# Performance work log

Measured on AMD Instinct MI355X. Metric: run time of the kernel, lower is better.

## Reference

```python
import jax, jax.numpy as jnp
import numpy as np

CUTOFF = 10.0
EPS_W = 1e-5
EPS_LN = 1e-5

def _silu(v):
    return v * jax.nn.sigmoid(v)

def setup_inputs() -> dict:
    key = jax.random.key(0)
    ks = jax.random.split(key, 12)
    N, E, H, R = 50000, 300000, 256, 64
    s = lambda fan_in: 1.0 / np.sqrt(fan_in)
    inp = {
        'x': jax.random.normal(ks[0], (N, H), jnp.float32),
        'edge_index': jax.random.randint(ks[1], (2, E), 0, N, jnp.int64 if jax.config.jax_enable_x64 else jnp.int32),
        'distances': jax.random.uniform(ks[2], (E,), jnp.float32) * CUTOFF,
        'centers': jnp.linspace(0.0, CUTOFF, R).astype(jnp.float32),
        'widths': jnp.full((R,), CUTOFF / R, jnp.float32),
        'rbf_w1': jax.random.normal(ks[3], (R, R), jnp.float32) * s(R),
        'rbf_b1': jnp.zeros((R,), jnp.float32),
        'rbf_w2': jax.random.normal(ks[4], (R, R), jnp.float32) * s(R),
        'rbf_b2': jnp.zeros((R,), jnp.float32),
        'filt_w1': jax.random.normal(ks[5], (R, H), jnp.float32) * s(R),
        'filt_b1': jnp.zeros((H,), jnp.float32),
        'filt_w2': jax.random.normal(ks[6], (H, H), jnp.float32) * s(H),
        'filt_b2': jnp.zeros((H,), jnp.float32),
        'filt_w3': jax.random.normal(ks[7], (H, H), jnp.float32) * s(H),
        'filt_b3': jnp.zeros((H,), jnp.float32),
        'node_w': jax.random.normal(ks[8], (H, H), jnp.float32) * s(H),
        'node_b': jnp.zeros((H,), jnp.float32),
        'ln_g': jnp.ones((H,), jnp.float32),
        'ln_b': jnp.zeros((H,), jnp.float32),
        'gate_w': jax.random.normal(ks[9], (H, H), jnp.float32) * s(H),
        'gate_b': jnp.zeros((H,), jnp.float32),
    }
    return inp

def reference(x, edge_index, distances, centers, widths,
              rbf_w1, rbf_b1, rbf_w2, rbf_b2,
              filt_w1, filt_b1, filt_w2, filt_b2, filt_w3, filt_b3,
              node_w, node_b, ln_g, ln_b, gate_w, gate_b):
    # LearnableRBF: envelope * gaussian basis, then 2-layer SiLU proj
    d = distances
    env = 0.5 * (jnp.cos(d * jnp.pi / CUTOFF) + 1.0) * (d < CUTOFF).astype(x.dtype)  # [E]
    rbf = jnp.exp(-0.5 * ((d[:, None] - centers) / (jnp.abs(widths) + EPS_W)) ** 2)   # [E,R]
    r = rbf * env[:, None]
    r = _silu(r @ rbf_w1 + rbf_b1) @ rbf_w2 + rbf_b2                                  # [E,R]
    # filter network: Lin-SiLU-Lin-SiLU-Lin
    W = _silu(r @ filt_w1 + filt_b1)
    W = _silu(W @ filt_w2 + filt_b2) @ filt_w3 + filt_b3                              # [E,H]
    # gather -> modulate -> scatter-add (CFConv messaging)
    row, col = edge_index[0], edge_index[1]
    msg = (x[col] @ node_w + node_b) * W                                              # [E,H]
    agg = jax.ops.segment_sum(msg, row, num_segments=x.shape[0])                      # [N,H]
    h = x + agg
    mu = jnp.mean(h, axis=-1, keepdims=True)
    var = jnp.var(h, axis=-1, keepdims=True)
    out = (h - mu) / jnp.sqrt(var + EPS_LN) * ln_g + ln_b
    return out * jax.nn.sigmoid(out @ gate_w + gate_b)
```

## Files before the change

### kernel.cpp

```cpp
#include <hip/hip_runtime.h>
#include <hip/hip_bf16.h>
#include <math.h>

typedef __attribute__((ext_vector_type(8))) short bf16x8;
typedef __attribute__((ext_vector_type(4))) float f32x4;
typedef unsigned short ushort_t;

constexpr float F_CUTOFF = 10.0f;
constexpr float F_EPS_W  = 1e-5f;
constexpr float F_EPS_LN = 1e-5f;
constexpr float F_PI     = 3.14159265358979323846f;

__device__ __forceinline__ float silu_f(float v)   { return v / (1.0f + __expf(-v)); }
__device__ __forceinline__ float sigmoid_f(float v){ return 1.0f / (1.0f + __expf(-v)); }

__device__ __forceinline__ ushort_t f2bf(float f) {
    union { __hip_bfloat16 h; ushort_t u; } v; v.h = __float2bfloat16(f); return v.u;
}
__device__ __forceinline__ float bf2f(ushort_t u) {
    union { unsigned u; float f; } v; v.u = ((unsigned)u) << 16; return v.f;
}

__device__ __forceinline__ float f4c(const float4& v, int q) {
    return q == 0 ? v.x : q == 1 ? v.y : q == 2 ? v.z : v.w;
}

__global__ void count_kernel(const int* __restrict__ eidx, int* __restrict__ cnt, int E)
{
    int e = blockIdx.x * 256 + threadIdx.x;
    if (e < E) atomicAdd(&cnt[eidx[e]], 1);
}

__global__ __launch_bounds__(1024)
void scan_kernel(int* __restrict__ cnt ,
                 int* __restrict__ start, int N)
{
    __shared__ int part[1024];
    const int tid = threadIdx.x;
    const int C = (N + 1023) >> 10;
    const int base = tid * C;
    int s = 0;
    for (int i = 0; i < C; ++i) {
        int idx = base + i;
        if (idx < N) s += cnt[idx];
    }
    part[tid] = s;
    __syncthreads();
    for (int off = 1; off < 1024; off <<= 1) {
        int v = (tid >= off) ? part[tid - off] : 0;
        __syncthreads();
        part[tid] += v;
        __syncthreads();
    }
    int run = part[tid] - s;
    for (int i = 0; i < C; ++i) {
        int idx = base + i;
        if (idx < N) {
            int c = cnt[idx];
            start[idx] = run;
            cnt[idx]   = run;
            run += c;
        }
    }
    if (tid == 1023) start[N] = part[1023];
}

__global__ void scatter_kernel(const int* __restrict__ eidx, int* __restrict__ cursor,
                               int* __restrict__ slot, int* __restrict__ colos, int E)
{
    int e = blockIdx.x * 256 + threadIdx.x;
    if (e < E) {
        int s = atomicAdd(&cursor[eidx[e]], 1);
        slot[e] = s;
        colos[s] = eidx[E + e];
    }
}

__global__ void cvt_transpose_kernel(const float* __restrict__ in, ushort_t* __restrict__ out,
                                     int K, int N, int logK)
{
    int idx = blockIdx.x * 256 + threadIdx.x;
    if (idx >= K * N) return;
    int n = idx >> logK;
    int k = idx & (K - 1);
    out[idx] = f2bf(in[k * N + n]);
}

__global__ void combine_w_kernel(const float* __restrict__ w2, const float* __restrict__ fw1,
                                 ushort_t* __restrict__ out)
{
    int idx = blockIdx.x * 256 + threadIdx.x;
    int c = idx >> 6, j = idx & 63;
    float s = 0.f;
    #pragma unroll 8
    for (int n = 0; n < 64; ++n) s += w2[j * 64 + n] * fw1[n * 256 + c];
    out[idx] = f2bf(s);
}

__global__ void combine_b_kernel(const float* __restrict__ b2, const float* __restrict__ fw1,
                                 const float* __restrict__ fb1, float* __restrict__ out)
{
    int c = threadIdx.x;
    float s = fb1[c];
    #pragma unroll 8
    for (int n = 0; n < 64; ++n) s += b2[n] * fw1[n * 256 + c];
    out[c] = s;
}

__global__ __launch_bounds__(256)
void gemm256_bf16_kernel(const float* __restrict__ A, const float* __restrict__ Wm,
                         const float* __restrict__ bias, ushort_t* __restrict__ out, int M)
{
    __shared__ float4 As4[64][64];
    const int t = threadIdx.x;
    const int row0 = blockIdx.x * 64;

    #pragma unroll
    for (int i = 0; i < 16; ++i) {
        int flat = t + i * 256;
        int r = flat >> 6, k4 = flat & 63;
        int row = row0 + r;
        float4 v = make_float4(0.f, 0.f, 0.f, 0.f);
        if (row < M) v = reinterpret_cast<const float4*>(A)[row * 64 + k4];
        As4[r][k4] = v;
    }
    __syncthreads();

    const int jt  = t & 31;
    const int et  = t >> 5;
    const int j04 = jt * 2;
    const int r0  = et * 8;

    float acc[8][8];
    #pragma unroll
    for (int r = 0; r < 8; ++r)
        #pragma unroll
        for (int c = 0; c < 8; ++c) acc[r][c] = 0.f;

    for (int k4 = 0; k4 < 64; ++k4) {
        float4 a4[8];
        #pragma unroll
        for (int r = 0; r < 8; ++r) a4[r] = As4[r0 + r][k4];
        #pragma unroll
        for (int q = 0; q < 4; ++q) {
            const int k = k4 * 4 + q;
            float4 b0 = reinterpret_cast<const float4*>(Wm)[k * 64 + j04];
            float4 b1 = reinterpret_cast<const float4*>(Wm)[k * 64 + j04 + 1];
            float bb[8] = {b0.x, b0.y, b0.z, b0.w, b1.x, b1.y, b1.z, b1.w};
            #pragma unroll
            for (int r = 0; r < 8; ++r) {
                float av = f4c(a4[r], q);
                #pragma unroll
                for (int c = 0; c < 8; ++c) acc[r][c] = fmaf(av, bb[c], acc[r][c]);
            }
        }
    }

    float4 bv0 = reinterpret_cast<const float4*>(bias)[j04];
    float4 bv1 = reinterpret_cast<const float4*>(bias)[j04 + 1];
    float bb[8] = {bv0.x, bv0.y, bv0.z, bv0.w, bv1.x, bv1.y, bv1.z, bv1.w};

    #pragma unroll
    for (int r = 0; r < 8; ++r) {
        int row = row0 + r0 + r;
        if (row >= M) continue;
        ushort_t o8[8];
        #pragma unroll
        for (int c = 0; c < 8; ++c) o8[c] = f2bf(acc[r][c] + bb[c]);
        *reinterpret_cast<uint4*>(out + (size_t)row * 256 + jt * 8) = *reinterpret_cast<uint4*>(o8);
    }
}

__global__ __launch_bounds__(256)
void gate_gemm_kernel(const float* __restrict__ A, const float* __restrict__ Wm,
                      const float* __restrict__ bias, float* __restrict__ out, int M)
{
    __shared__ float4 As4[64][64];
    const int t = threadIdx.x;
    const int row0 = blockIdx.x * 64;

    #pragma unroll
    for (int i = 0; i < 16; ++i) {
        int flat = t + i * 256;
        int r = flat >> 6, k4 = flat & 63;
        int row = row0 + r;
        float4 v = make_float4(0.f, 0.f, 0.f, 0.f);
        if (row < M) v = reinterpret_cast<const float4*>(A)[row * 64 + k4];
        As4[r][k4] = v;
    }
    __syncthreads();

    const int jt  = t & 31;
    const int et  = t >> 5;
    const int j04 = jt * 2;
    const int r0  = et * 8;

    float acc[8][8];
    #pragma unroll
    for (int r = 0; r < 8; ++r)
        #pragma unroll
        for (int c = 0; c < 8; ++c) acc[r][c] = 0.f;

    for (int k4 = 0; k4 < 64; ++k4) {
        float4 a4[8];
        #pragma unroll
        for (int r = 0; r < 8; ++r) a4[r] = As4[r0 + r][k4];
        #pragma unroll
        for (int q = 0; q < 4; ++q) {
            const int k = k4 * 4 + q;
            float4 b0 = reinterpret_cast<const float4*>(Wm)[k * 64 + j04];
            float4 b1 = reinterpret_cast<const float4*>(Wm)[k * 64 + j04 + 1];
            float bb[8] = {b0.x, b0.y, b0.z, b0.w, b1.x, b1.y, b1.z, b1.w};
            #pragma unroll
            for (int r = 0; r < 8; ++r) {
                float av = f4c(a4[r], q);
                #pragma unroll
                for (int c = 0; c < 8; ++c) acc[r][c] = fmaf(av, bb[c], acc[r][c]);
            }
        }
    }

    float4 bv0 = reinterpret_cast<const float4*>(bias)[j04];
    float4 bv1 = reinterpret_cast<const float4*>(bias)[j04 + 1];
    float bb[8] = {bv0.x, bv0.y, bv0.z, bv0.w, bv1.x, bv1.y, bv1.z, bv1.w};

    #pragma unroll
    for (int r = 0; r < 8; ++r) {
        int row = row0 + r0 + r;
        if (row >= M) continue;
        float4 a0 = As4[r0 + r][j04];
        float4 a1 = As4[r0 + r][j04 + 1];
        float aa[8] = {a0.x, a0.y, a0.z, a0.w, a1.x, a1.y, a1.z, a1.w};
        float o[8];
        #pragma unroll
        for (int c = 0; c < 8; ++c) o[c] = aa[c] * sigmoid_f(acc[r][c] + bb[c]);
        reinterpret_cast<float4*>(out)[row * 64 + j04]     = make_float4(o[0], o[1], o[2], o[3]);
        reinterpret_cast<float4*>(out)[row * 64 + j04 + 1] = make_float4(o[4], o[5], o[6], o[7]);
    }
}

template<int KS, int NT, bool SILU>
__device__ __forceinline__ void mlp_stage(const unsigned char* in, unsigned char* out,
                                          const ushort_t* __restrict__ Wt,
                                          const float* __restrict__ bias,
                                          int wn, int g, int q)
{
    constexpr int K = KS * 32;
    f32x4 acc[2][NT];
    #pragma unroll
    for (int mt = 0; mt < 2; ++mt)
        #pragma unroll
        for (int nt = 0; nt < NT; ++nt) acc[mt][nt] = (f32x4){0.f, 0.f, 0.f, 0.f};

    #pragma unroll
    for (int kk = 0; kk < KS; ++kk) {
        bf16x8 b[NT];
        #pragma unroll
        for (int nt = 0; nt < NT; ++nt) {
            int n = (wn * NT + nt) * 16 + q;
            b[nt] = *reinterpret_cast<const bf16x8*>(Wt + n * K + kk * 32 + g * 8);
        }
        bf16x8 a[2];
        #pragma unroll
        for (int mt = 0; mt < 2; ++mt) {
            int m = mt * 16 + q;
            int unit = (4 * kk + g) ^ (m & 7);
            a[mt] = *reinterpret_cast<const bf16x8*>(in + m * 512 + unit * 16);
        }
        #pragma unroll
        for (int mt = 0; mt < 2; ++mt)
            #pragma unroll
            for (int nt = 0; nt < NT; ++nt)
                acc[mt][nt] = __builtin_amdgcn_mfma_f32_16x16x32_bf16(a[mt], b[nt], acc[mt][nt], 0, 0, 0);
    }

    const bool evenq = (q & 1) == 0;
    #pragma unroll
    for (int nt = 0; nt < NT; ++nt) {
        int n0  = (wn * NT + nt) * 16 + q;
        int n_e = n0 & ~1;
        float2 bv = *reinterpret_cast<const float2*>(bias + n_e);
        #pragma unroll
        for (int mt = 0; mt < 2; ++mt) {
            float v[4], p[4];
            #pragma unroll
            for (int r = 0; r < 4; ++r) { v[r] = acc[mt][nt][r]; p[r] = __shfl_xor(v[r], 1, 64); }
            #pragma unroll
            for (int rr = 0; rr < 2; ++rr) {
                int r = evenq ? rr : (2 + rr);
                float lo = (evenq ? v[r] : p[r]) + bv.x;
                float hi = (evenq ? p[r] : v[r]) + bv.y;
                if (SILU) { lo = silu_f(lo); hi = silu_f(hi); }
                int m = mt * 16 + 4 * g + r;
                unsigned u = (unsigned)f2bf(lo) | ((unsigned)f2bf(hi) << 16);
                int byte = m * 512 + (((n_e >> 3) ^ (m & 7)) << 4) + ((n_e & 7) * 2);
                *reinterpret_cast<unsigned*>(out + byte) = u;
            }
        }
    }
}

__global__ __launch_bounds__(256, 4)
void rbf_f1_kernel(const float* __restrict__ dist,
                   const float* __restrict__ centers, const float* __restrict__ widths,
                   const ushort_t* __restrict__ wt_rbf1, const float* __restrict__ rbf_b1,
                   const ushort_t* __restrict__ wt_comb, const float* __restrict__ b_comb,
                   ushort_t* __restrict__ f1, int E)
{
    __shared__ __align__(16) unsigned char bufA[16384];
    __shared__ __align__(16) unsigned char bufB[16384];

    const int t  = threadIdx.x;
    const int e0 = blockIdx.x * 32;
    const int wn   = t >> 6;
    const int lane = t & 63;
    const int g = lane >> 4, q = lane & 15;

    const int e_own  = t >> 3;
    const int chunk  = t & 7;
    const int ge_own = e0 + e_own;

    {
        float d = (ge_own < E) ? dist[ge_own] : F_CUTOFF;
        float env = (d < F_CUTOFF) ? 0.5f * (__cosf(d * (F_PI / F_CUTOFF)) + 1.0f) : 0.0f;
        unsigned char* rowp = bufA + e_own * 512;
        int k0 = chunk * 8;
        #pragma unroll
        for (int i = 0; i < 4; ++i) {
            int n = k0 + 2 * i;
            float c0 = centers[n],     w0 = fabsf(widths[n]) + F_EPS_W;
            float c1 = centers[n + 1], w1 = fabsf(widths[n + 1]) + F_EPS_W;
            float z0 = (d - c0) / w0, z1 = (d - c1) / w1;
            float r0 = env * __expf(-0.5f * z0 * z0);
            float r1 = env * __expf(-0.5f * z1 * z1);
            unsigned u = (unsigned)f2bf(r0) | ((unsigned)f2bf(r1) << 16);
            int byte = (((n >> 3) ^ (e_own & 7)) << 4) + ((n & 7) * 2);
            *reinterpret_cast<unsigned*>(rowp + byte) = u;
        }
    }
    __syncthreads();

    mlp_stage<2, 1, true>(bufA, bufB, wt_rbf1, rbf_b1, wn, g, q);
    __syncthreads();
    mlp_stage<2, 4, true>(bufB, bufA, wt_comb, b_comb, wn, g, q);
    __syncthreads();

    if (ge_own < E) {
        #pragma unroll
        for (int i = 0; i < 4; ++i) {
            int c = chunk + i * 8;
            int u = (c ^ (e_own & 7)) | (c & 24);
            u = (c & 24) | ((c ^ (e_own & 7)) & 7);
            uint4 v = *reinterpret_cast<const uint4*>(bufA + e_own * 512 + u * 16);
            *reinterpret_cast<uint4*>(f1 + (size_t)ge_own * 256 + c * 8) = v;
        }
    }
}

template<int EPI>
__global__ __launch_bounds__(256, 3)
void gemm_stage_kernel(const ushort_t* __restrict__ A, const ushort_t* __restrict__ Wt,
                       const float* __restrict__ bias, ushort_t* __restrict__ out,
                       const int* __restrict__ slot, int M)
{
    __shared__ __align__(16) unsigned char sbuf[2][8192];
    __shared__ int slot_s[64];

    const int t  = threadIdx.x;
    const int m0 = blockIdx.x * 64;
    const int wn   = t >> 6;
    const int lane = t & 63;
    const int g = lane >> 4, q = lane & 15;

    if (EPI == 1 && t < 64) {
        int gm = m0 + t;
        slot_s[t] = (gm < M) ? slot[gm] : 0;
    }

    const int s0r = t >> 3,        s0u = t & 7;
    const int s1r = (t + 256) >> 3, s1u = t & 7;
    const ushort_t* src0base = A + (size_t)((m0 + s0r < M) ? (m0 + s0r) : (M - 1)) * 256 + ((s0u ^ (s0r & 7)) * 8);
    const ushort_t* src1base = A + (size_t)((m0 + s1r < M) ? (m0 + s1r) : (M - 1)) * 256 + ((s1u ^ (s1r & 7)) * 8);

    uint4 p0 = *reinterpret_cast<const uint4*>(src0base);
    uint4 p1 = *reinterpret_cast<const uint4*>(src1base);
    *reinterpret_cast<uint4*>(&sbuf[0][t * 16])         = p0;
    *reinterpret_cast<uint4*>(&sbuf[0][(t + 256) * 16]) = p1;
    __syncthreads();

    f32x4 acc[4][4];
    #pragma unroll
    for (int mt = 0; mt < 4; ++mt)
        #pragma unroll
        for (int nt = 0; nt < 4; ++nt) acc[mt][nt] = (f32x4){0.f, 0.f, 0.f, 0.f};

    for (int kt = 0; kt < 4; ++kt) {
        const int cur = kt & 1;
        uint4 nx0, nx1;
        if (kt < 3) {
            nx0 = *reinterpret_cast<const uint4*>(src0base + (kt + 1) * 64);
            nx1 = *reinterpret_cast<const uint4*>(src1base + (kt + 1) * 64);
        }
        #pragma unroll
        for (int ks = 0; ks < 2; ++ks) {
            bf16x8 b[4];
            #pragma unroll
            for (int nt = 0; nt < 4; ++nt) {
                int n = wn * 64 + nt * 16 + q;
                b[nt] = *reinterpret_cast<const bf16x8*>(Wt + (size_t)n * 256 + kt * 64 + ks * 32 + g * 8);
            }
            bf16x8 a[4];
            #pragma unroll
            for (int mt = 0; mt < 4; ++mt) {
                int r = mt * 16 + q;
                int u = (ks * 4 + g) ^ (r & 7);
                a[mt] = *reinterpret_cast<const bf16x8*>(&sbuf[cur][r * 128 + u * 16]);
            }
            #pragma unroll
            for (int mt = 0; mt < 4; ++mt)
                #pragma unroll
                for (int nt = 0; nt < 4; ++nt)
                    acc[mt][nt] = __builtin_amdgcn_mfma_f32_16x16x32_bf16(a[mt], b[nt], acc[mt][nt], 0, 0, 0);
        }
        __syncthreads();
        if (kt < 3) {
            *reinterpret_cast<uint4*>(&sbuf[cur ^ 1][t * 16])         = nx0;
            *reinterpret_cast<uint4*>(&sbuf[cur ^ 1][(t + 256) * 16]) = nx1;
            __syncthreads();
        }
    }

    const bool evenq = (q & 1) == 0;
    #pragma unroll
    for (int nt = 0; nt < 4; ++nt) {
        int n0  = wn * 64 + nt * 16 + q;
        int n_e = n0 & ~1;
        float2 bv = *reinterpret_cast<const float2*>(bias + n_e);
        #pragma unroll
        for (int mt = 0; mt < 4; ++mt) {
            float v[4], p[4];
            #pragma unroll
            for (int r = 0; r < 4; ++r) { v[r] = acc[mt][nt][r]; p[r] = __shfl_xor(v[r], 1, 64); }
            #pragma unroll
            for (int rr = 0; rr < 2; ++rr) {
                int r = evenq ? rr : (2 + rr);
                float lo = (evenq ? v[r] : p[r]) + bv.x;
                float hi = (evenq ? p[r] : v[r]) + bv.y;
                if (EPI == 0) { lo = silu_f(lo); hi = silu_f(hi); }
                int mloc = mt * 16 + 4 * g + r;
                int grow = m0 + mloc;
                if (grow < M) {
                    int drow = (EPI == 1) ? slot_s[mloc] : grow;
                    unsigned u = (unsigned)f2bf(lo) | ((unsigned)f2bf(hi) << 16);
                    *reinterpret_cast<unsigned*>(out + (size_t)drow * 256 + n_e) = u;
                }
            }
        }
    }
}

__global__ __launch_bounds__(256)
void agg_ln2_kernel(const float* __restrict__ x, const ushort_t* __restrict__ Wf,
                    const int* __restrict__ start, const int* __restrict__ colos,
                    const ushort_t* __restrict__ y,
                    const float* __restrict__ g, const float* __restrict__ b,
                    float* __restrict__ out0, int N)
{
    int lane = threadIdx.x & 63;
    int row  = blockIdx.x * 4 + (threadIdx.x >> 6);
    if (row >= N) return;
    int s0 = start[row], s1 = start[row + 1];
    float4 hx = reinterpret_cast<const float4*>(x)[row * 64 + lane];
    float hh[4] = {hx.x, hx.y, hx.z, hx.w};
    for (int s = s0; s < s1; ++s) {
        uint2 wv = *reinterpret_cast<const uint2*>(Wf + (size_t)s * 256 + lane * 4);
        int c = colos[s];
        uint2 yv = *reinterpret_cast<const uint2*>(y + (size_t)c * 256 + lane * 4);
        hh[0] += bf2f((ushort_t)(wv.x & 0xffff)) * bf2f((ushort_t)(yv.x & 0xffff));
        hh[1] += bf2f((ushort_t)(wv.x >> 16))    * bf2f((ushort_t)(yv.x >> 16));
        hh[2] += bf2f((ushort_t)(wv.y & 0xffff)) * bf2f((ushort_t)(yv.y & 0xffff));
        hh[3] += bf2f((ushort_t)(wv.y >> 16))    * bf2f((ushort_t)(yv.y >> 16));
    }
    float su = hh[0] + hh[1] + hh[2] + hh[3];
    float s2 = hh[0]*hh[0] + hh[1]*hh[1] + hh[2]*hh[2] + hh[3]*hh[3];
    #pragma unroll
    for (int off = 32; off > 0; off >>= 1) {
        su += __shfl_xor(su, off, 64);
        s2 += __shfl_xor(s2, off, 64);
    }
    float mu  = su * (1.0f / 256.0f);
    float var = s2 * (1.0f / 256.0f) - mu * mu;
    float inv = rsqrtf(var + F_EPS_LN);
    float4 gv = reinterpret_cast<const float4*>(g)[lane];
    float4 bv = reinterpret_cast<const float4*>(b)[lane];
    float4 o;
    o.x = (hh[0] - mu) * inv * gv.x + bv.x;
    o.y = (hh[1] - mu) * inv * gv.y + bv.y;
    o.z = (hh[2] - mu) * inv * gv.z + bv.z;
    o.w = (hh[3] - mu) * inv * gv.w + bv.w;
    reinterpret_cast<float4*>(out0)[row * 64 + lane] = o;
}

__global__ __launch_bounds__(256, 4)
void edge_atomic_kernel(const float* __restrict__ dist, const int* __restrict__ eidx,
                        const float* __restrict__ centers, const float* __restrict__ widths,
                        const ushort_t* __restrict__ wt_rbf1, const float* __restrict__ rbf_b1,
                        const ushort_t* __restrict__ wt_comb, const float* __restrict__ b_comb,
                        const ushort_t* __restrict__ wt_f2, const float* __restrict__ filt_b2,
                        const ushort_t* __restrict__ wt_f3, const float* __restrict__ filt_b3,
                        const ushort_t* __restrict__ y, float* __restrict__ agg, int E)
{
    __shared__ __align__(16) unsigned char bufA[16384];
    __shared__ __align__(16) unsigned char bufB[16384];
    __shared__ int rs_s[32];

    const int t  = threadIdx.x;
    const int e0 = blockIdx.x * 32;
    const int wn   = t >> 6;
    const int lane = t & 63;
    const int g = lane >> 4, q = lane & 15;

    if (t < 32) {
        int ge = e0 + t;
        rs_s[t] = (ge < E) ? eidx[ge] : 0;
    }

    const int e_own  = t >> 3;
    const int chunk  = t & 7;
    const int ge_own = e0 + e_own;
    const int col_own = (ge_own < E) ? eidx[E + ge_own] : 0;
    uint4 yv[4];
    #pragma unroll
    for (int i = 0; i < 4; ++i)
        yv[i] = *reinterpret_cast<const uint4*>(y + (size_t)col_own * 256 + (i * 8 + chunk) * 8);

    {
        float d = (ge_own < E) ? dist[ge_own] : F_CUTOFF;
        float env = (d < F_CUTOFF) ? 0.5f * (__cosf(d * (F_PI / F_CUTOFF)) + 1.0f) : 0.0f;
        unsigned char* rowp = bufA + e_own * 512;
        int k0 = chunk * 8;
        #pragma unroll
        for (int i = 0; i < 4; ++i) {
            int n = k0 + 2 * i;
            float c0 = centers[n],     w0 = fabsf(widths[n]) + F_EPS_W;
            float c1 = centers[n + 1], w1 = fabsf(widths[n + 1]) + F_EPS_W;
            float z0 = (d - c0) / w0, z1 = (d - c1) / w1;
            float r0 = env * __expf(-0.5f * z0 * z0);
            float r1 = env * __expf(-0.5f * z1 * z1);
            unsigned u = (unsigned)f2bf(r0) | ((unsigned)f2bf(r1) << 16);
            int byte = (((n >> 3) ^ (e_own & 7)) << 4) + ((n & 7) * 2);
            *reinterpret_cast<unsigned*>(rowp + byte) = u;
        }
    }
    __syncthreads();

    mlp_stage<2, 1, true>(bufA, bufB, wt_rbf1, rbf_b1, wn, g, q);
    __syncthreads();
    mlp_stage<2, 4, true>(bufB, bufA, wt_comb, b_comb, wn, g, q);
    __syncthreads();
    mlp_stage<8, 4, true>(bufA, bufB, wt_f2, filt_b2, wn, g, q);
    __syncthreads();

    #pragma unroll
    for (int i = 0; i < 4; ++i)
        *reinterpret_cast<uint4*>(bufA + e_own * 512 + (i * 8 + chunk) * 16) = yv[i];
    __syncthreads();

    {
        f32x4 acc[2][4];
        #pragma unroll
        for (int mt = 0; mt < 2; ++mt)
            #pragma unroll
            for (int nt = 0; nt < 4; ++nt) acc[mt][nt] = (f32x4){0.f, 0.f, 0.f, 0.f};

        #pragma unroll
        for (int kk = 0; kk < 8; ++kk) {
            bf16x8 b[4];
            #pragma unroll
            for (int nt = 0; nt < 4; ++nt) {
                int n = (wn * 4 + nt) * 16 + q;
                b[nt] = *reinterpret_cast<const bf16x8*>(wt_f3 + n * 256 + kk * 32 + g * 8);
            }
            bf16x8 a[2];
            #pragma unroll
            for (int mt = 0; mt < 2; ++mt) {
                int m = mt * 16 + q;
                int unit = (4 * kk + g) ^ (m & 7);
                a[mt] = *reinterpret_cast<const bf16x8*>(bufB + m * 512 + unit * 16);
            }
            #pragma unroll
            for (int mt = 0; mt < 2; ++mt)
                #pragma unroll
                for (int nt = 0; nt < 4; ++nt)
                    acc[mt][nt] = __builtin_amdgcn_mfma_f32_16x16x32_bf16(a[mt], b[nt], acc[mt][nt], 0, 0, 0);
        }

        float bn[4];
        int   nn[4];
        #pragma unroll
        for (int nt = 0; nt < 4; ++nt) { nn[nt] = (wn * 4 + nt) * 16 + q; bn[nt] = filt_b3[nn[nt]]; }

        #pragma unroll
        for (int mt = 0; mt < 2; ++mt) {
            #pragma unroll
            for (int r = 0; r < 4; ++r) {
                int m  = mt * 16 + 4 * g + r;
                int ge = e0 + m;
                if (ge < E) {
                    const unsigned char* yrow = bufA + m * 512;
                    float* arow = agg + (size_t)rs_s[m] * 256;
                    #pragma unroll
                    for (int nt = 0; nt < 4; ++nt) {
                        float wv = acc[mt][nt][r] + bn[nt];
                        float yvv = bf2f(*reinterpret_cast<const ushort_t*>(yrow + nn[nt] * 2));
                        unsafeAtomicAdd(&arow[nn[nt]], wv * yvv);
                    }
                }
            }
        }
    }
}

__global__ __launch_bounds__(256)
void ln_kernel(const float* __restrict__ x, const float* __restrict__ agg,
               const float* __restrict__ g, const float* __restrict__ b,
               float* __restrict__ out0, int N)
{
    int lane = threadIdx.x & 63;
    int row  = blockIdx.x * 4 + (threadIdx.x >> 6);
    if (row >= N) return;
    float4 hx = reinterpret_cast<const float4*>(x)[row * 64 + lane];
    float4 ha = reinterpret_cast<const float4*>(agg)[row * 64 + lane];
    float4 h  = make_float4(hx.x + ha.x, hx.y + ha.y, hx.z + ha.z, hx.w + ha.w);
    float s  = h.x + h.y + h.z + h.w;
    float s2 = h.x * h.x + h.y * h.y + h.z * h.z + h.w * h.w;
    #pragma unroll
    for (int off = 32; off > 0; off >>= 1) {
        s  += __shfl_xor(s,  off, 64);
        s2 += __shfl_xor(s2, off, 64);
    }
    float mu  = s * (1.0f / 256.0f);
    float var = s2 * (1.0f / 256.0f) - mu * mu;
    float inv = rsqrtf(var + F_EPS_LN);
    float4 gv = reinterpret_cast<const float4*>(g)[lane];
    float4 bv = reinterpret_cast<const float4*>(b)[lane];
    float4 o;
    o.x = (h.x - mu) * inv * gv.x + bv.x;
    o.y = (h.y - mu) * inv * gv.y + bv.y;
    o.z = (h.z - mu) * inv * gv.z + bv.z;
    o.w = (h.w - mu) * inv * gv.w + bv.w;
    reinterpret_cast<float4*>(out0)[row * 64 + lane] = o;
}

extern "C" void kernel_launch(void* const* d_in, const int* in_sizes, int n_in,
                              void* d_out, int out_size, void* d_ws, size_t ws_size,
                              hipStream_t stream)
{
    const float* x       = (const float*)d_in[0];
    const int*   eidx    = (const int*)  d_in[1];
    const float* dist    = (const float*)d_in[2];
    const float* centers = (const float*)d_in[3];
    const float* widths  = (const float*)d_in[4];
    const float* rbf_w1  = (const float*)d_in[5];
    const float* rbf_b1  = (const float*)d_in[6];
    const float* rbf_w2  = (const float*)d_in[7];
    const float* rbf_b2  = (const float*)d_in[8];
    const float* filt_w1 = (const float*)d_in[9];
    const float* filt_b1 = (const float*)d_in[10];
    const float* filt_w2 = (const float*)d_in[11];
    const float* filt_b2 = (const float*)d_in[12];
    const float* filt_w3 = (const float*)d_in[13];
    const float* filt_b3 = (const float*)d_in[14];
    const float* node_w  = (const float*)d_in[15];
    const float* node_b  = (const float*)d_in[16];
    const float* ln_g    = (const float*)d_in[17];
    const float* ln_b    = (const float*)d_in[18];
    const float* gate_w  = (const float*)d_in[19];
    const float* gate_b  = (const float*)d_in[20];

    const int N = in_sizes[0] / 256;
    const int E = in_sizes[2];

    char* wsb = (char*)d_ws;
    size_t off = 0;
    auto alloc = [&](size_t bytes, size_t align) -> char* {
        off = (off + align - 1) & ~(align - 1);
        char* p = wsb + off;
        off += bytes;
        return p;
    };
    ushort_t* y_bf  = (ushort_t*)alloc((size_t)N * 256 * 2, 16);
    ushort_t* wt1   = (ushort_t*)alloc(64 * 64 * 2, 16);
    ushort_t* wcomb = (ushort_t*)alloc(256 * 64 * 2, 16);
    ushort_t* wf2t  = (ushort_t*)alloc(256 * 256 * 2, 16);
    ushort_t* wf3t  = (ushort_t*)alloc(256 * 256 * 2, 16);
    float*    bcomb = (float*)   alloc(256 * 4, 16);
    int*      cnt   = (int*)     alloc((size_t)N * 4, 16);
    int*      start = (int*)     alloc(((size_t)N + 1) * 4, 16);
    int*      slot  = (int*)     alloc((size_t)E * 4, 16);
    int*      colos = (int*)     alloc((size_t)E * 4, 16);
    ushort_t* f1    = (ushort_t*)alloc((size_t)E * 256 * 2, 1024);
    ushort_t* f2    = (ushort_t*)alloc((size_t)E * 256 * 2, 1024);
    ushort_t* Wf    = f1;
    const bool two_phase = (off <= ws_size);

    dim3 b256(256);

    cvt_transpose_kernel<<<dim3((64 * 64 + 255) / 256),   b256, 0, stream>>>(rbf_w1,  wt1, 64, 64, 6);
    combine_w_kernel<<<dim3(64), b256, 0, stream>>>(rbf_w2, filt_w1, wcomb);
    combine_b_kernel<<<dim3(1), b256, 0, stream>>>(rbf_b2, filt_w1, filt_b1, bcomb);
    cvt_transpose_kernel<<<dim3((256 * 256 + 255) / 256), b256, 0, stream>>>(filt_w2, wf2t, 256, 256, 8);
    cvt_transpose_kernel<<<dim3((256 * 256 + 255) / 256), b256, 0, stream>>>(filt_w3, wf3t, 256, 256, 8);

    gemm256_bf16_kernel<<<dim3((N + 63) / 64), b256, 0, stream>>>(x, node_w, node_b, y_bf, N);

    if (two_phase) {
        hipMemsetAsync(cnt, 0, (size_t)N * 4, stream);
        count_kernel<<<dim3((E + 255) / 256), b256, 0, stream>>>(eidx, cnt, E);
        scan_kernel<<<dim3(1), 1024, 0, stream>>>(cnt, start, N);
        scatter_kernel<<<dim3((E + 255) / 256), b256, 0, stream>>>(eidx, cnt, slot, colos, E);

        rbf_f1_kernel<<<dim3((E + 31) / 32), b256, 0, stream>>>(
            dist, centers, widths, wt1, rbf_b1, wcomb, bcomb, f1, E);

        gemm_stage_kernel<0><<<dim3((E + 63) / 64), b256, 0, stream>>>(
            f1, wf2t, filt_b2, f2, nullptr, E);

        gemm_stage_kernel<1><<<dim3((E + 63) / 64), b256, 0, stream>>>(
            f2, wf3t, filt_b3, Wf, slot, E);

        agg_ln2_kernel<<<dim3((N + 3) / 4), b256, 0, stream>>>(
            x, Wf, start, colos, y_bf, ln_g, ln_b, (float*)d_out, N);
    } else {
        hipMemsetAsync(d_out, 0, (size_t)out_size * sizeof(float), stream);
        edge_atomic_kernel<<<dim3((E + 31) / 32), b256, 0, stream>>>(
            dist, eidx, centers, widths,
            wt1, rbf_b1, wcomb, bcomb,
            wf2t, filt_b2, wf3t, filt_b3,
            y_bf, (float*)d_out, E);
        ln_kernel<<<dim3((N + 3) / 4), b256, 0, stream>>>(x, (float*)d_out, ln_g, ln_b, (float*)d_out, N);
    }

    gate_gemm_kernel<<<dim3((N + 63) / 64), b256, 0, stream>>>((float*)d_out, gate_w, gate_b, (float*)d_out, N);
}
```

Before: 822.8 us.

## Fuse edge filter MLP and scatter into one CSR-sorted kernel

Replaces the multi-kernel two-phase path, which wrote f1/f2 edge intermediates to global memory and then ran a separate CSR aggregation, with a single edge kernel. Edges are pre-permuted into destination-sorted order along with their distances and node ids. The kernel runs all filter MLP stages in shared memory, multiplies by the gathered node features, and reduces consecutive same-destination rows within the block. It writes directly when a node's edges fall entirely inside the block and uses atomics otherwise. This removes roughly E*256*2 bytes of intermediate traffic per stage at the cost of atomics, a memset, and a separate LN pass.

```diff
diff --git a/kernel.cpp b/kernel.cpp
--- a/kernel.cpp
+++ b/kernel.cpp
@@ -65,14 +65,18 @@
     if (tid == 1023) start[N] = part[1023];
 }
 
-__global__ void scatter_kernel(const int* __restrict__ eidx, int* __restrict__ cursor,
-                               int* __restrict__ slot, int* __restrict__ colos, int E)
+__global__ void scatter_kernel(const int* __restrict__ eidx, const float* __restrict__ dist,
+                               int* __restrict__ cursor,
+                               int* __restrict__ colp, int* __restrict__ nodep,
+                               float* __restrict__ distp, int E)
 {
     int e = blockIdx.x * 256 + threadIdx.x;
     if (e < E) {
-        int s = atomicAdd(&cursor[eidx[e]], 1);
-        slot[e] = s;
-        colos[s] = eidx[E + e];
+        int row = eidx[e];
+        int s = atomicAdd(&cursor[row], 1);
+        colp[s]  = eidx[E + e];
+        nodep[s] = row;
+        distp[s] = dist[e];
     }
 }
 
@@ -301,14 +305,20 @@
 }
 
 __global__ __launch_bounds__(256, 4)
-void rbf_f1_kernel(const float* __restrict__ dist,
-                   const float* __restrict__ centers, const float* __restrict__ widths,
-                   const ushort_t* __restrict__ wt_rbf1, const float* __restrict__ rbf_b1,
-                   const ushort_t* __restrict__ wt_comb, const float* __restrict__ b_comb,
-                   ushort_t* __restrict__ f1, int E)
-{
-    __shared__ __align__(16) unsigned char bufA[16384];
-    __shared__ __align__(16) unsigned char bufB[16384];
+void edge_csr_kernel(const float* __restrict__ distp, const int* __restrict__ colp,
+                     const int* __restrict__ nodep, const int* __restrict__ start,
+                     const float* __restrict__ centers, const float* __restrict__ widths,
+                     const ushort_t* __restrict__ wt_rbf1, const float* __restrict__ rbf_b1,
+                     const ushort_t* __restrict__ wt_comb, const float* __restrict__ b_comb,
+                     const ushort_t* __restrict__ wt_f2, const float* __restrict__ filt_b2,
+                     const ushort_t* __restrict__ wt_f3, const float* __restrict__ filt_b3,
+                     const ushort_t* __restrict__ y, float* __restrict__ agg, int E)
+{
+    __shared__ __align__(16) unsigned char buf[32768];
+    __shared__ int node_s[32];
+    __shared__ int flag_s[32];
+    unsigned char* bufA = buf;
+    unsigned char* bufB = buf + 16384;
 
     const int t  = threadIdx.x;
     const int e0 = blockIdx.x * 32;
@@ -316,12 +326,29 @@
     const int lane = t & 63;
     const int g = lane >> 4, q = lane & 15;
 
+    if (t < 32) {
+        int ge = e0 + t;
+        int nd = (ge < E) ? nodep[ge] : -1;
+        node_s[t] = nd;
+        int fl = 0;
+        if (nd >= 0) {
+            int lo = start[nd], hi = start[nd + 1];
+            fl = (lo >= e0 && hi <= e0 + 32) ? 1 : 0;
+        }
+        flag_s[t] = fl;
+    }
+
     const int e_own  = t >> 3;
     const int chunk  = t & 7;
     const int ge_own = e0 + e_own;
+    const int col_own = (ge_own < E) ? colp[ge_own] : 0;
+    uint4 yv[4];
+    #pragma unroll
+    for (int i = 0; i < 4; ++i)
+        yv[i] = *reinterpret_cast<const uint4*>(y + (size_t)col_own * 256 + (i * 8 + chunk) * 8);
 
     {
-        float d = (ge_own < E) ? dist[ge_own] : F_CUTOFF;
+        float d = (ge_own < E) ? distp[ge_own] : F_CUTOFF;
         float env = (d < F_CUTOFF) ? 0.5f * (__cosf(d * (F_PI / F_CUTOFF)) + 1.0f) : 0.0f;
         unsigned char* rowp = bufA + e_own * 512;
         int k0 = chunk * 8;
@@ -344,161 +371,97 @@
     __syncthreads();
     mlp_stage<2, 4, true>(bufB, bufA, wt_comb, b_comb, wn, g, q);
     __syncthreads();
-
-    if (ge_own < E) {
-        #pragma unroll
-        for (int i = 0; i < 4; ++i) {
-            int c = chunk + i * 8;
-            int u = (c ^ (e_own & 7)) | (c & 24);
-            u = (c & 24) | ((c ^ (e_own & 7)) & 7);
-            uint4 v = *reinterpret_cast<const uint4*>(bufA + e_own * 512 + u * 16);
-            *reinterpret_cast<uint4*>(f1 + (size_t)ge_own * 256 + c * 8) = v;
-        }
-    }
-}
-
-template<int EPI>
-__global__ __launch_bounds__(256, 3)
-void gemm_stage_kernel(const ushort_t* __restrict__ A, const ushort_t* __restrict__ Wt,
-                       const float* __restrict__ bias, ushort_t* __restrict__ out,
-                       const int* __restrict__ slot, int M)
-{
-    __shared__ __align__(16) unsigned char sbuf[2][8192];
-    __shared__ int slot_s[64];
-
-    const int t  = threadIdx.x;
-    const int m0 = blockIdx.x * 64;
-    const int wn   = t >> 6;
-    const int lane = t & 63;
-    const int g = lane >> 4, q = lane & 15;
-
-    if (EPI == 1 && t < 64) {
-        int gm = m0 + t;
-        slot_s[t] = (gm < M) ? slot[gm] : 0;
-    }
-
-    const int s0r = t >> 3,        s0u = t & 7;
-    const int s1r = (t + 256) >> 3, s1u = t & 7;
-    const ushort_t* src0base = A + (size_t)((m0 + s0r < M) ? (m0 + s0r) : (M - 1)) * 256 + ((s0u ^ (s0r & 7)) * 8);
-    const ushort_t* src1base = A + (size_t)((m0 + s1r < M) ? (m0 + s1r) : (M - 1)) * 256 + ((s1u ^ (s1r & 7)) * 8);
-
-    uint4 p0 = *reinterpret_cast<const uint4*>(src0base);
-    uint4 p1 = *reinterpret_cast<const uint4*>(src1base);
-    *reinterpret_cast<uint4*>(&sbuf[0][t * 16])         = p0;
-    *reinterpret_cast<uint4*>(&sbuf[0][(t + 256) * 16]) = p1;
-    __syncthreads();
-
-    f32x4 acc[4][4];
-    #pragma unroll
-    for (int mt = 0; mt < 4; ++mt)
+    mlp_stage<8, 4, true>(bufA, bufB, wt_f2, filt_b2, wn, g, q);
+    __syncthreads();
+
+    #pragma unroll
+    for (int i = 0; i < 4; ++i)
+        *reinterpret_cast<uint4*>(bufA + e_own * 512 + (i * 8 + chunk) * 16) = yv[i];
+    __syncthreads();
+
+    f32x4 acc[2][4];
+    #pragma unroll
+    for (int mt = 0; mt < 2; ++mt)
         #pragma unroll
         for (int nt = 0; nt < 4; ++nt) acc[mt][nt] = (f32x4){0.f, 0.f, 0.f, 0.f};
 
-    for (int kt = 0; kt < 4; ++kt) {
-        const int cur = kt & 1;
-        uint4 nx0, nx1;
-        if (kt < 3) {
-            nx0 = *reinterpret_cast<const uint4*>(src0base + (kt + 1) * 64);
-            nx1 = *reinterpret_cast<const uint4*>(src1base + (kt + 1) * 64);
-        }
-        #pragma unroll
-        for (int ks = 0; ks < 2; ++ks) {
-            bf16x8 b[4];
+    #pragma unroll
+    for (int kk = 0; kk < 8; ++kk) {
+        bf16x8 b[4];
+        #pragma unroll
+        for (int nt = 0; nt < 4; ++nt) {
+            int n = (wn * 4 + nt) * 16 + q;
+            b[nt] = *reinterpret_cast<const bf16x8*>(wt_f3 + n * 256 + kk * 32 + g * 8);
+        }
+        bf16x8 a[2];
+        #pragma unroll
+        for (int mt = 0; mt < 2; ++mt) {
+            int m = mt * 16 + q;
+            int unit = (4 * kk + g) ^ (m & 7);
+            a[mt] = *reinterpret_cast<const bf16x8*>(bufB + m * 512 + unit * 16);
+        }
+        #pragma unroll
+        for (int mt = 0; mt < 2; ++mt)
+            #pragma unroll
+            for (int nt = 0; nt < 4; ++nt)
+                acc[mt][nt] = __builtin_amdgcn_mfma_f32_16x16x32_bf16(a[mt], b[nt], acc[mt][nt], 0, 0, 0);
+    }
+
+    float bn[4];
+    int   nn[4];
+    #pragma unroll
+    for (int nt = 0; nt < 4; ++nt) { nn[nt] = (wn * 4 + nt) * 16 + q; bn[nt] = filt_b3[nn[nt]]; }
+
+    #pragma unroll
+    for (int mt = 0; mt < 2; ++mt) {
+        #pragma unroll
+        for (int r = 0; r < 4; ++r) {
+            int m = mt * 16 + 4 * g + r;
+            const unsigned char* yrow = bufA + m * 512;
             #pragma unroll
             for (int nt = 0; nt < 4; ++nt) {
-                int n = wn * 64 + nt * 16 + q;
-                b[nt] = *reinterpret_cast<const bf16x8*>(Wt + (size_t)n * 256 + kt * 64 + ks * 32 + g * 8);
+                float yvv = bf2f(*reinterpret_cast<const ushort_t*>(yrow + nn[nt] * 2));
+                acc[mt][nt][r] = (acc[mt][nt][r] + bn[nt]) * yvv;
             }
-            bf16x8 a[4];
-            #pragma unroll
-            for (int mt = 0; mt < 4; ++mt) {
-                int r = mt * 16 + q;
-                int u = (ks * 4 + g) ^ (r & 7);
-                a[mt] = *reinterpret_cast<const bf16x8*>(&sbuf[cur][r * 128 + u * 16]);
+        }
+    }
+    __syncthreads();
+
+    float* msgf = reinterpret_cast<float*>(buf);
+    #pragma unroll
+    for (int mt = 0; mt < 2; ++mt) {
+        #pragma unroll
+        for (int r = 0; r < 4; ++r) {
+            int m  = mt * 16 + 4 * g + r;
+            #pragma unroll
+            for (int nt = 0; nt < 4; ++nt)
+                msgf[m * 256 + nn[nt]] = acc[mt][nt][r];
+        }
+    }
+    __syncthreads();
+
+    {
+        const int j = t;
+        float accv = 0.f;
+        int cur = -2, rs = 0;
+        #pragma unroll 4
+        for (int r = 0; r < 32; ++r) {
+            int nd = node_s[r];
+            if (nd != cur) {
+                if (cur >= 0) {
+                    if (flag_s[rs]) agg[(size_t)cur * 256 + j] = accv;
+                    else            unsafeAtomicAdd(&agg[(size_t)cur * 256 + j], accv);
+                }
+                cur = nd; rs = r; accv = msgf[r * 256 + j];
+            } else {
+                accv += msgf[r * 256 + j];
             }
-            #pragma unroll
-            for (int mt = 0; mt < 4; ++mt)
-                #pragma unroll
-                for (int nt = 0; nt < 4; ++nt)
-                    acc[mt][nt] = __builtin_amdgcn_mfma_f32_16x16x32_bf16(a[mt], b[nt], acc[mt][nt], 0, 0, 0);
-        }
-        __syncthreads();
-        if (kt < 3) {
-            *reinterpret_cast<uint4*>(&sbuf[cur ^ 1][t * 16])         = nx0;
-            *reinterpret_cast<uint4*>(&sbuf[cur ^ 1][(t + 256) * 16]) = nx1;
-            __syncthreads();
-        }
-    }
-
-    const bool evenq = (q & 1) == 0;
-    #pragma unroll
-    for (int nt = 0; nt < 4; ++nt) {
-        int n0  = wn * 64 + nt * 16 + q;
-        int n_e = n0 & ~1;
-        float2 bv = *reinterpret_cast<const float2*>(bias + n_e);
-        #pragma unroll
-        for (int mt = 0; mt < 4; ++mt) {
-            float v[4], p[4];
-            #pragma unroll
-            for (int r = 0; r < 4; ++r) { v[r] = acc[mt][nt][r]; p[r] = __shfl_xor(v[r], 1, 64); }
-            #pragma unroll
-            for (int rr = 0; rr < 2; ++rr) {
-                int r = evenq ? rr : (2 + rr);
-                float lo = (evenq ? v[r] : p[r]) + bv.x;
-                float hi = (evenq ? p[r] : v[r]) + bv.y;
-                if (EPI == 0) { lo = silu_f(lo); hi = silu_f(hi); }
-                int mloc = mt * 16 + 4 * g + r;
-                int grow = m0 + mloc;
-                if (grow < M) {
-                    int drow = (EPI == 1) ? slot_s[mloc] : grow;
-                    unsigned u = (unsigned)f2bf(lo) | ((unsigned)f2bf(hi) << 16);
-                    *reinterpret_cast<unsigned*>(out + (size_t)drow * 256 + n_e) = u;
-                }
-            }
-        }
-    }
-}
-
-__global__ __launch_bounds__(256)
-void agg_ln2_kernel(const float* __restrict__ x, const ushort_t* __restrict__ Wf,
-                    const int* __restrict__ start, const int* __restrict__ colos,
-                    const ushort_t* __restrict__ y,
-                    const float* __restrict__ g, const float* __restrict__ b,
-                    float* __restrict__ out0, int N)
-{
-    int lane = threadIdx.x & 63;
-    int row  = blockIdx.x * 4 + (threadIdx.x >> 6);
-    if (row >= N) return;
-    int s0 = start[row], s1 = start[row + 1];
-    float4 hx = reinterpret_cast<const float4*>(x)[row * 64 + lane];
-    float hh[4] = {hx.x, hx.y, hx.z, hx.w};
-    for (int s = s0; s < s1; ++s) {
-        uint2 wv = *reinterpret_cast<const uint2*>(Wf + (size_t)s * 256 + lane * 4);
-        int c = colos[s];
-        uint2 yv = *reinterpret_cast<const uint2*>(y + (size_t)c * 256 + lane * 4);
-        hh[0] += bf2f((ushort_t)(wv.x & 0xffff)) * bf2f((ushort_t)(yv.x & 0xffff));
-        hh[1] += bf2f((ushort_t)(wv.x >> 16))    * bf2f((ushort_t)(yv.x >> 16));
-        hh[2] += bf2f((ushort_t)(wv.y & 0xffff)) * bf2f((ushort_t)(yv.y & 0xffff));
-        hh[3] += bf2f((ushort_t)(wv.y >> 16))    * bf2f((ushort_t)(yv.y >> 16));
-    }
-    float su = hh[0] + hh[1] + hh[2] + hh[3];
-    float s2 = hh[0]*hh[0] + hh[1]*hh[1] + hh[2]*hh[2] + hh[3]*hh[3];
-    #pragma unroll
-    for (int off = 32; off > 0; off >>= 1) {
-        su += __shfl_xor(su, off, 64);
-        s2 += __shfl_xor(s2, off, 64);
-    }
-    float mu  = su * (1.0f / 256.0f);
-    float var = s2 * (1.0f / 256.0f) - mu * mu;
-    float inv = rsqrtf(var + F_EPS_LN);
-    float4 gv = reinterpret_cast<const float4*>(g)[lane];
-    float4 bv = reinterpret_cast<const float4*>(b)[lane];
-    float4 o;
-    o.x = (hh[0] - mu) * inv * gv.x + bv.x;
-    o.y = (hh[1] - mu) * inv * gv.y + bv.y;
-    o.z = (hh[2] - mu) * inv * gv.z + bv.z;
-    o.w = (hh[3] - mu) * inv * gv.w + bv.w;
-    reinterpret_cast<float4*>(out0)[row * 64 + lane] = o;
+        }
+        if (cur >= 0) {
+            if (flag_s[rs]) agg[(size_t)cur * 256 + j] = accv;
+            else            unsafeAtomicAdd(&agg[(size_t)cur * 256 + j], accv);
+        }
+    }
 }
 
 __global__ __launch_bounds__(256, 4)
@@ -697,12 +660,10 @@
     float*    bcomb = (float*)   alloc(256 * 4, 16);
     int*      cnt   = (int*)     alloc((size_t)N * 4, 16);
     int*      start = (int*)     alloc(((size_t)N + 1) * 4, 16);
-    int*      slot  = (int*)     alloc((size_t)E * 4, 16);
-    int*      colos = (int*)     alloc((size_t)E * 4, 16);
-    ushort_t* f1    = (ushort_t*)alloc((size_t)E * 256 * 2, 1024);
-    ushort_t* f2    = (ushort_t*)alloc((size_t)E * 256 * 2, 1024);
-    ushort_t* Wf    = f1;
-    const bool two_phase = (off <= ws_size);
+    int*      colp  = (int*)     alloc((size_t)E * 4, 16);
+    int*      nodep = (int*)     alloc((size_t)E * 4, 16);
+    float*    distp = (float*)   alloc((size_t)E * 4, 16);
+    const bool csr_fits = (off <= ws_size);
 
     dim3 b256(256);
 
@@ -714,32 +675,27 @@
 
     gemm256_bf16_kernel<<<dim3((N + 63) / 64), b256, 0, stream>>>(x, node_w, node_b, y_bf, N);
 
-    if (two_phase) {
+    hipMemsetAsync(d_out, 0, (size_t)out_size * sizeof(float), stream);
+
+    if (csr_fits) {
         hipMemsetAsync(cnt, 0, (size_t)N * 4, stream);
         count_kernel<<<dim3((E + 255) / 256), b256, 0, stream>>>(eidx, cnt, E);
         scan_kernel<<<dim3(1), 1024, 0, stream>>>(cnt, start, N);
-        scatter_kernel<<<dim3((E + 255) / 256), b256, 0, stream>>>(eidx, cnt, slot, colos, E);
-
-        rbf_f1_kernel<<<dim3((E + 31) / 32), b256, 0, stream>>>(
-            dist, centers, widths, wt1, rbf_b1, wcomb, bcomb, f1, E);
-
-        gemm_stage_kernel<0><<<dim3((E + 63) / 64), b256, 0, stream>>>(
-            f1, wf2t, filt_b2, f2, nullptr, E);
-
-        gemm_stage_kernel<1><<<dim3((E + 63) / 64), b256, 0, stream>>>(
-            f2, wf3t, filt_b3, Wf, slot, E);
-
-        agg_ln2_kernel<<<dim3((N + 3) / 4), b256, 0, stream>>>(
-            x, Wf, start, colos, y_bf, ln_g, ln_b, (float*)d_out, N);
+        scatter_kernel<<<dim3((E + 255) / 256), b256, 0, stream>>>(eidx, dist, cnt, colp, nodep, distp, E);
+
+        edge_csr_kernel<<<dim3((E + 31) / 32), b256, 0, stream>>>(
+            distp, colp, nodep, start, centers, widths,
+            wt1, rbf_b1, wcomb, bcomb,
+            wf2t, filt_b2, wf3t, filt_b3,
+            y_bf, (float*)d_out, E);
     } else {
-        hipMemsetAsync(d_out, 0, (size_t)out_size * sizeof(float), stream);
         edge_atomic_kernel<<<dim3((E + 31) / 32), b256, 0, stream>>>(
             dist, eidx, centers, widths,
             wt1, rbf_b1, wcomb, bcomb,
             wf2t, filt_b2, wf3t, filt_b3,
             y_bf, (float*)d_out, E);
-        ln_kernel<<<dim3((N + 3) / 4), b256, 0, stream>>>(x, (float*)d_out, ln_g, ln_b, (float*)d_out, N);
-    }
-
+    }
+
+    ln_kernel<<<dim3((N + 3) / 4), b256, 0, stream>>>(x, (float*)d_out, ln_g, ln_b, (float*)d_out, N);
     gate_gemm_kernel<<<dim3((N + 63) / 64), b256, 0, stream>>>((float*)d_out, gate_w, gate_b, (float*)d_out, N);
 }
```

Result: slower. 948.0 us (+15.2%).
